# Optimization experiments

Measured on AMD Instinct MI355X. Metric: run time of the kernel, lower is better.

## Reference

```python
import jax, jax.numpy as jnp
import numpy as np
from jax import lax

FILTERS = 8      # Conv1D filters per column
K = 5            # kernel_size
ACTION_DIM = 2
COLS = [16, 128, 1024]  # columns entering each of the 3 blocks (grow x FILTERS)


def setup_inputs() -> dict:
    key = jax.random.key(0)
    ks = jax.random.split(key, 8)
    B, L, C = 64, 128, 16
    state = jax.random.normal(ks[0], (B, L, C), jnp.float32)
    inp = {"state": state}
    # One grouped-conv kernel per block: WIO layout [K, in_per_group=1, cols*FILTERS].
    # Channel c*FILTERS+f of the output is column c's filter f (matches Keras concat order).
    for i, c in enumerate(COLS):
        inp[f"k{i+1}"] = jax.random.normal(ks[1 + i], (K, 1, c * FILTERS), jnp.float32) * 0.1
        inp[f"b{i+1}"] = jnp.zeros((c * FILTERS,), jnp.float32)
    L_final = L - len(COLS) * (K - 1)          # 116
    feat = L_final * COLS[-1] * FILTERS        # 950272
    inp["W"] = jax.random.normal(ks[4], (feat, ACTION_DIM), jnp.float32) * 1e-3
    inp["bd"] = jnp.zeros((ACTION_DIM,), jnp.float32)
    return inp


def _block(x, kern, bias):
    # x: [B, cols, L]  ->  [B, cols*FILTERS, L-K+1]
    cols = x.shape[1]
    xin = jnp.transpose(x, (0, 2, 1))  # [B, L, cols] (NWC)
    y = lax.conv_general_dilated(
        xin, kern, window_strides=(1,), padding='VALID',
        dimension_numbers=('NWC', 'WIO', 'NWC'), feature_group_count=cols)
    y = jax.nn.relu(y + bias)          # [B, L', cols*FILTERS]
    return jnp.transpose(y, (0, 2, 1))


def reference(state, k1, b1, k2, b2, k3, b3, W, bd):
    # Actor.call: transpose [B,L,C] -> [B,C,L], run blocks, transpose back, flatten, dense+tanh
    x = jnp.transpose(state, (0, 2, 1))  # [B, cols=16, L=128]
    for kern, bias in ((k1, b1), (k2, b2), (k3, b3)):
        x = _block(x, kern, bias)
    x = jnp.transpose(x, (0, 2, 1)).reshape(state.shape[0], -1)  # [B, L'*channels]
    return jnp.tanh(x @ W + bd)  # [B, ACTION_DIM]
```

## Files before the change

### kernel.cpp

```cpp
#include <hip/hip_runtime.h>
#include <math.h>

#define NB    64
#define L0    128
#define C0    16
#define KW    5
#define NF    8
#define L1    124
#define L2    120
#define L3    116
#define CH1   128
#define CH2   1024
#define CH3   8192
#define NCHUNK 8
#define NS     4
#define SLICE  29
#define TROWS  (SLICE + 4)
#define Y1R    (SLICE + 8)
#define STR    (SLICE + 12)
#define NFH    4
#define NBATCH 4
#define NBG    (NB / NBATCH)

__global__ __launch_bounds__(256, 2) void actor_fused_kernel(
    const float* __restrict__ state,
    const float* __restrict__ k1,
    const float* __restrict__ b1,
    const float* __restrict__ k2,
    const float* __restrict__ b2,
    const float* __restrict__ k3,
    const float* __restrict__ b3,
    const float* __restrict__ W,
    float* __restrict__ partials)
{
    const int chunk = blockIdx.x;
    const int bg    = blockIdx.y;
    const int slice = blockIdx.z;
    const int t0    = slice * SLICE;
    const int tid   = threadIdx.x;
    const int c3loc = tid >> 1;
    const int fh    = tid & 1;
    const int c3    = chunk * 128 + c3loc;

    __shared__ float s_state[NBATCH][STR][2];
    __shared__ float s_y1[NBATCH][Y1R][16];
    __shared__ float tile[NBATCH][TROWS][128];

    {
        int bb = tid >> 6, lt = tid & 63;
        const float* sp = state + (size_t)(bg * NBATCH + bb) * L0 * C0
                        + (size_t)t0 * C0 + chunk * 2;
        for (int i = lt; i < STR * 2; i += 64) {
            int r = i >> 1, c = i & 1;
            s_state[bb][r][c] = sp[r * C0 + c];
        }
    }
    __syncthreads();

    {
        int bb = tid >> 6, lt = tid & 63;
        for (int i = lt; i < Y1R * 16; i += 64) {
            int r = i >> 4, jloc = i & 15;
            int j = chunk * 16 + jloc;
            int cloc = jloc >> 3;
            float acc = b1[j];
#pragma unroll
            for (int k = 0; k < KW; ++k)
                acc = fmaf(s_state[bb][r + k][cloc], k1[k * CH1 + j], acc);
            s_y1[bb][r][jloc] = fmaxf(acc, 0.f);
        }
    }
    __syncthreads();

    {
        int c = tid & 127, h = tid >> 7;
        int m = chunk * 128 + c;
        int jloc = c >> 3;
        float kk[KW], b2v = b2[m];
#pragma unroll
        for (int k = 0; k < KW; ++k) kk[k] = k2[k * CH2 + m];
        int r0 = h ? 17 : 0, r1 = h ? TROWS : 17;
#pragma unroll
        for (int bb = 0; bb < NBATCH; ++bb)
            for (int r = r0; r < r1; ++r) {
                float acc = b2v;
#pragma unroll
                for (int k = 0; k < KW; ++k)
                    acc = fmaf(s_y1[bb][r + k][jloc], kk[k], acc);
                tile[bb][r][c] = fmaxf(acc, 0.f);
            }
    }

    float kw[KW][NFH], bv[NFH];
#pragma unroll
    for (int k = 0; k < KW; ++k)
#pragma unroll
        for (int f = 0; f < NFH; ++f)
            kw[k][f] = k3[k * CH3 + c3 * NF + fh * NFH + f];
#pragma unroll
    for (int f = 0; f < NFH; ++f)
        bv[f] = b3[c3 * NF + fh * NFH + f];

    __syncthreads();

    float ax[NBATCH], ay[NBATCH];
#pragma unroll
    for (int bb = 0; bb < NBATCH; ++bb) { ax[bb] = 0.f; ay[bb] = 0.f; }

    float w[NBATCH][4];
#pragma unroll
    for (int bb = 0; bb < NBATCH; ++bb)
#pragma unroll
        for (int r = 0; r < 4; ++r)
            w[bb][r] = tile[bb][r][c3loc];

    const float4* __restrict__ wp =
        (const float4*)W + (size_t)t0 * 4096 + (size_t)c3 * 4 + fh * 2;

    for (int t = 0; t < SLICE; ++t) {
        float4 q0 = wp[0];
        float4 q1 = wp[1];
        wp += 4096;

        float v[NBATCH][NFH];
#pragma unroll
        for (int bb = 0; bb < NBATCH; ++bb) {
            float w4 = tile[bb][t + 4][c3loc];
#pragma unroll
            for (int f = 0; f < NFH; ++f) {
                float a = bv[f];
                a = fmaf(w[bb][0], kw[0][f], a);
                a = fmaf(w[bb][1], kw[1][f], a);
                a = fmaf(w[bb][2], kw[2][f], a);
                a = fmaf(w[bb][3], kw[3][f], a);
                a = fmaf(w4,       kw[4][f], a);
                v[bb][f] = fmaxf(a, 0.f);
            }
            w[bb][0] = w[bb][1]; w[bb][1] = w[bb][2];
            w[bb][2] = w[bb][3]; w[bb][3] = w4;
        }

#pragma unroll
        for (int bb = 0; bb < NBATCH; ++bb) {
            ax[bb] = fmaf(v[bb][0], q0.x, ax[bb]); ay[bb] = fmaf(v[bb][0], q0.y, ay[bb]);
            ax[bb] = fmaf(v[bb][1], q0.z, ax[bb]); ay[bb] = fmaf(v[bb][1], q0.w, ay[bb]);
            ax[bb] = fmaf(v[bb][2], q1.x, ax[bb]); ay[bb] = fmaf(v[bb][2], q1.y, ay[bb]);
            ax[bb] = fmaf(v[bb][3], q1.z, ax[bb]); ay[bb] = fmaf(v[bb][3], q1.w, ay[bb]);
        }
    }

#pragma unroll
    for (int bb = 0; bb < NBATCH; ++bb) {
#pragma unroll
        for (int d = 32; d >= 1; d >>= 1) {
            ax[bb] += __shfl_down(ax[bb], d, 64);
            ay[bb] += __shfl_down(ay[bb], d, 64);
        }
    }
    __shared__ float red[4][NBATCH][2];
    int wave = tid >> 6, lane = tid & 63;
    if (lane == 0) {
#pragma unroll
        for (int bb = 0; bb < NBATCH; ++bb) {
            red[wave][bb][0] = ax[bb];
            red[wave][bb][1] = ay[bb];
        }
    }
    __syncthreads();
    if (tid < NBATCH * 2) {
        int bb = tid >> 1, a = tid & 1;
        float s = (red[0][bb][a] + red[1][bb][a]) + (red[2][bb][a] + red[3][bb][a]);
        int b = bg * NBATCH + bb;
        partials[(((size_t)b * NCHUNK + chunk) * NS + slice) * 2 + a] = s;
    }
}

__global__ __launch_bounds__(128) void finish_kernel(
    const float* __restrict__ partials,
    const float* __restrict__ bd,
    float* __restrict__ out)
{
    int i = threadIdx.x;
    int b = i >> 1, a = i & 1;
    float s = bd[a];
#pragma unroll
    for (int p = 0; p < NCHUNK * NS; ++p)
        s += partials[((size_t)b * NCHUNK * NS + p) * 2 + a];
    out[b * 2 + a] = tanhf(s);
}

extern "C" void kernel_launch(void* const* d_in, const int* in_sizes, int n_in,
                              void* d_out, int out_size, void* d_ws, size_t ws_size,
                              hipStream_t stream) {
    const float* state = (const float*)d_in[0];
    const float* k1    = (const float*)d_in[1];
    const float* b1    = (const float*)d_in[2];
    const float* k2    = (const float*)d_in[3];
    const float* b2    = (const float*)d_in[4];
    const float* k3    = (const float*)d_in[5];
    const float* b3    = (const float*)d_in[6];
    const float* W     = (const float*)d_in[7];
    const float* bd    = (const float*)d_in[8];
    float* out = (float*)d_out;

    float* partials = (float*)d_ws;

    dim3 grid(NCHUNK, NBG, NS);
    actor_fused_kernel<<<grid, 256, 0, stream>>>(
        state, k1, b1, k2, b2, k3, b3, W, partials);

    finish_kernel<<<1, 128, 0, stream>>>(partials, bd, out);
}
```

Baseline: 93.06 us.

## Interleave batch dimension into float4 shared-memory tiles and prefetch W one step ahead

Shared-memory tiles now store the four batches of each position as one float4, so layer-2 and layer-3 loops do one 128-bit LDS per row instead of four scalar loads. The batch loop becomes float4 arithmetic, and sliding-window registers are kept across rows in layer 2. The W loads for the next time step are issued one iteration early to hide global-memory latency. The cost is higher per-thread register use, which may pressure the 2-blocks-per-CU occupancy target, and possible bank conflicts on the wider shared-memory accesses.

Result: no change. 92.71 us (-0.4%).

```diff
diff --git a/kernel.cpp b/kernel.cpp
--- a/kernel.cpp
+++ b/kernel.cpp
@@ -6,9 +6,6 @@
 #define C0    16
 #define KW    5
 #define NF    8
-#define L1    124
-#define L2    120
-#define L3    116
 #define CH1   128
 #define CH2   1024
 #define CH3   8192
@@ -21,6 +18,16 @@
 #define NFH    4
 #define NBATCH 4
 #define NBG    (NB / NBATCH)
+
+__device__ __forceinline__ float4 fma4(float4 a, float s, float4 c) {
+    return make_float4(fmaf(a.x, s, c.x), fmaf(a.y, s, c.y),
+                       fmaf(a.z, s, c.z), fmaf(a.w, s, c.w));
+}
+__device__ __forceinline__ float4 relu4(float4 a) {
+    return make_float4(fmaxf(a.x, 0.f), fmaxf(a.y, 0.f),
+                       fmaxf(a.z, 0.f), fmaxf(a.w, 0.f));
+}
+__device__ __forceinline__ float4 splat4(float s) { return make_float4(s, s, s, s); }
 
 __global__ __launch_bounds__(256, 2) void actor_fused_kernel(
     const float* __restrict__ state,
@@ -42,9 +49,9 @@
     const int fh    = tid & 1;
     const int c3    = chunk * 128 + c3loc;
 
-    __shared__ float s_state[NBATCH][STR][2];
-    __shared__ float s_y1[NBATCH][Y1R][16];
-    __shared__ float tile[NBATCH][TROWS][128];
+    __shared__ float  s_state[NBATCH][STR][2];
+    __shared__ float4 s_y1[Y1R][16];
+    __shared__ float4 tile[TROWS][128];
 
     {
         int bb = tid >> 6, lt = tid & 63;
@@ -67,7 +74,7 @@
 #pragma unroll
             for (int k = 0; k < KW; ++k)
                 acc = fmaf(s_state[bb][r + k][cloc], k1[k * CH1 + j], acc);
-            s_y1[bb][r][jloc] = fmaxf(acc, 0.f);
+            ((float*)&s_y1[r][jloc])[bb] = fmaxf(acc, 0.f);
         }
     }
     __syncthreads();
@@ -80,15 +87,21 @@
 #pragma unroll
         for (int k = 0; k < KW; ++k) kk[k] = k2[k * CH2 + m];
         int r0 = h ? 17 : 0, r1 = h ? TROWS : 17;
-#pragma unroll
-        for (int bb = 0; bb < NBATCH; ++bb)
-            for (int r = r0; r < r1; ++r) {
-                float acc = b2v;
-#pragma unroll
-                for (int k = 0; k < KW; ++k)
-                    acc = fmaf(s_y1[bb][r + k][jloc], kk[k], acc);
-                tile[bb][r][c] = fmaxf(acc, 0.f);
-            }
+        float4 u0 = s_y1[r0 + 0][jloc];
+        float4 u1 = s_y1[r0 + 1][jloc];
+        float4 u2 = s_y1[r0 + 2][jloc];
+        float4 u3 = s_y1[r0 + 3][jloc];
+        for (int r = r0; r < r1; ++r) {
+            float4 u4 = s_y1[r + 4][jloc];
+            float4 acc = splat4(b2v);
+            acc = fma4(u0, kk[0], acc);
+            acc = fma4(u1, kk[1], acc);
+            acc = fma4(u2, kk[2], acc);
+            acc = fma4(u3, kk[3], acc);
+            acc = fma4(u4, kk[4], acc);
+            tile[r][c] = relu4(acc);
+            u0 = u1; u1 = u2; u2 = u3; u3 = u4;
+        }
     }
 
     float kw[KW][NFH], bv[NFH];
@@ -103,68 +116,59 @@
 
     __syncthreads();
 
-    float ax[NBATCH], ay[NBATCH];
-#pragma unroll
-    for (int bb = 0; bb < NBATCH; ++bb) { ax[bb] = 0.f; ay[bb] = 0.f; }
-
-    float w[NBATCH][4];
-#pragma unroll
-    for (int bb = 0; bb < NBATCH; ++bb)
-#pragma unroll
-        for (int r = 0; r < 4; ++r)
-            w[bb][r] = tile[bb][r][c3loc];
-
-    const float4* __restrict__ wp =
+    float4 axv = splat4(0.f), ayv = splat4(0.f);
+
+    const float4* __restrict__ wq =
         (const float4*)W + (size_t)t0 * 4096 + (size_t)c3 * 4 + fh * 2;
+    float4 cq0 = wq[0];
+    float4 cq1 = wq[1];
+
+    float4 tw0 = tile[0][c3loc];
+    float4 tw1 = tile[1][c3loc];
+    float4 tw2 = tile[2][c3loc];
+    float4 tw3 = tile[3][c3loc];
 
     for (int t = 0; t < SLICE; ++t) {
-        float4 q0 = wp[0];
-        float4 q1 = wp[1];
-        wp += 4096;
-
-        float v[NBATCH][NFH];
-#pragma unroll
-        for (int bb = 0; bb < NBATCH; ++bb) {
-            float w4 = tile[bb][t + 4][c3loc];
-#pragma unroll
-            for (int f = 0; f < NFH; ++f) {
-                float a = bv[f];
-                a = fmaf(w[bb][0], kw[0][f], a);
-                a = fmaf(w[bb][1], kw[1][f], a);
-                a = fmaf(w[bb][2], kw[2][f], a);
-                a = fmaf(w[bb][3], kw[3][f], a);
-                a = fmaf(w4,       kw[4][f], a);
-                v[bb][f] = fmaxf(a, 0.f);
-            }
-            w[bb][0] = w[bb][1]; w[bb][1] = w[bb][2];
-            w[bb][2] = w[bb][3]; w[bb][3] = w4;
-        }
-
-#pragma unroll
-        for (int bb = 0; bb < NBATCH; ++bb) {
-            ax[bb] = fmaf(v[bb][0], q0.x, ax[bb]); ay[bb] = fmaf(v[bb][0], q0.y, ay[bb]);
-            ax[bb] = fmaf(v[bb][1], q0.z, ax[bb]); ay[bb] = fmaf(v[bb][1], q0.w, ay[bb]);
-            ax[bb] = fmaf(v[bb][2], q1.x, ax[bb]); ay[bb] = fmaf(v[bb][2], q1.y, ay[bb]);
-            ax[bb] = fmaf(v[bb][3], q1.z, ax[bb]); ay[bb] = fmaf(v[bb][3], q1.w, ay[bb]);
-        }
-    }
-
-#pragma unroll
-    for (int bb = 0; bb < NBATCH; ++bb) {
-#pragma unroll
-        for (int d = 32; d >= 1; d >>= 1) {
-            ax[bb] += __shfl_down(ax[bb], d, 64);
-            ay[bb] += __shfl_down(ay[bb], d, 64);
-        }
+        float4 tw4 = tile[t + 4][c3loc];
+        int tp = (t < SLICE - 1) ? (t + 1) : (SLICE - 1);
+        float4 nq0 = wq[(size_t)tp * 4096];
+        float4 nq1 = wq[(size_t)tp * 4096 + 1];
+
+        float4 v[NFH];
+#pragma unroll
+        for (int f = 0; f < NFH; ++f) {
+            float4 a = splat4(bv[f]);
+            a = fma4(tw0, kw[0][f], a);
+            a = fma4(tw1, kw[1][f], a);
+            a = fma4(tw2, kw[2][f], a);
+            a = fma4(tw3, kw[3][f], a);
+            a = fma4(tw4, kw[4][f], a);
+            v[f] = relu4(a);
+        }
+
+        axv = fma4(v[0], cq0.x, axv); ayv = fma4(v[0], cq0.y, ayv);
+        axv = fma4(v[1], cq0.z, axv); ayv = fma4(v[1], cq0.w, ayv);
+        axv = fma4(v[2], cq1.x, axv); ayv = fma4(v[2], cq1.y, ayv);
+        axv = fma4(v[3], cq1.z, axv); ayv = fma4(v[3], cq1.w, ayv);
+
+        cq0 = nq0; cq1 = nq1;
+        tw0 = tw1; tw1 = tw2; tw2 = tw3; tw3 = tw4;
+    }
+
+#pragma unroll
+    for (int d = 32; d >= 1; d >>= 1) {
+        axv.x += __shfl_down(axv.x, d, 64); ayv.x += __shfl_down(ayv.x, d, 64);
+        axv.y += __shfl_down(axv.y, d, 64); ayv.y += __shfl_down(ayv.y, d, 64);
+        axv.z += __shfl_down(axv.z, d, 64); ayv.z += __shfl_down(ayv.z, d, 64);
+        axv.w += __shfl_down(axv.w, d, 64); ayv.w += __shfl_down(ayv.w, d, 64);
     }
     __shared__ float red[4][NBATCH][2];
     int wave = tid >> 6, lane = tid & 63;
     if (lane == 0) {
-#pragma unroll
-        for (int bb = 0; bb < NBATCH; ++bb) {
-            red[wave][bb][0] = ax[bb];
-            red[wave][bb][1] = ay[bb];
-        }
+        red[wave][0][0] = axv.x; red[wave][0][1] = ayv.x;
+        red[wave][1][0] = axv.y; red[wave][1][1] = ayv.y;
+        red[wave][2][0] = axv.z; red[wave][2][1] = ayv.z;
+        red[wave][3][0] = axv.w; red[wave][3][1] = ayv.w;
     }
     __syncthreads();
     if (tid < NBATCH * 2) {
```

## Interleave batch in shared memory as float4 and software-pipeline W loads

Applied to the files above, without the earlier changes.

Shared-memory buffers are re-laid out so the four batch rows of each position sit together as one 4-wide vector. Each conv step then does a single vector LDS read and packed vector FMAs, which could map to the MI355X packed-FP32 instructions. The main loop is unrolled by two, with register rotation, and W loads are prefetched one iteration ahead to hide global latency. The costs are higher register pressure under launch_bounds(256,2) and more complex clamped index logic at the tail.

Result: faster. 90.03 us (median of 2 runs) (-3.3%).

```diff
diff --git a/kernel.cpp b/kernel.cpp
--- a/kernel.cpp
+++ b/kernel.cpp
@@ -6,9 +6,6 @@
 #define C0    16
 #define KW    5
 #define NF    8
-#define L1    124
-#define L2    120
-#define L3    116
 #define CH1   128
 #define CH2   1024
 #define CH3   8192
@@ -21,6 +18,16 @@
 #define NFH    4
 #define NBATCH 4
 #define NBG    (NB / NBATCH)
+
+typedef float v4f __attribute__((ext_vector_type(4)));
+
+__device__ __forceinline__ v4f splat(float s) { return (v4f){s, s, s, s}; }
+__device__ __forceinline__ v4f vfma(v4f a, float s, v4f c) {
+    return __builtin_elementwise_fma(a, splat(s), c);
+}
+__device__ __forceinline__ v4f vrelu(v4f a) {
+    return __builtin_elementwise_max(a, splat(0.f));
+}
 
 __global__ __launch_bounds__(256, 2) void actor_fused_kernel(
     const float* __restrict__ state,
@@ -43,8 +50,8 @@
     const int c3    = chunk * 128 + c3loc;
 
     __shared__ float s_state[NBATCH][STR][2];
-    __shared__ float s_y1[NBATCH][Y1R][16];
-    __shared__ float tile[NBATCH][TROWS][128];
+    __shared__ v4f   s_y1[Y1R][16];
+    __shared__ v4f   tile[TROWS][128];
 
     {
         int bb = tid >> 6, lt = tid & 63;
@@ -67,7 +74,7 @@
 #pragma unroll
             for (int k = 0; k < KW; ++k)
                 acc = fmaf(s_state[bb][r + k][cloc], k1[k * CH1 + j], acc);
-            s_y1[bb][r][jloc] = fmaxf(acc, 0.f);
+            ((float*)&s_y1[r][jloc])[bb] = fmaxf(acc, 0.f);
         }
     }
     __syncthreads();
@@ -79,16 +86,22 @@
         float kk[KW], b2v = b2[m];
 #pragma unroll
         for (int k = 0; k < KW; ++k) kk[k] = k2[k * CH2 + m];
-        int r0 = h ? 17 : 0, r1 = h ? TROWS : 17;
-#pragma unroll
-        for (int bb = 0; bb < NBATCH; ++bb)
-            for (int r = r0; r < r1; ++r) {
-                float acc = b2v;
-#pragma unroll
-                for (int k = 0; k < KW; ++k)
-                    acc = fmaf(s_y1[bb][r + k][jloc], kk[k], acc);
-                tile[bb][r][c] = fmaxf(acc, 0.f);
-            }
+        int r0i = h ? 17 : 0, r1i = h ? TROWS : 17;
+        v4f u0 = s_y1[r0i + 0][jloc];
+        v4f u1 = s_y1[r0i + 1][jloc];
+        v4f u2 = s_y1[r0i + 2][jloc];
+        v4f u3 = s_y1[r0i + 3][jloc];
+        for (int r = r0i; r < r1i; ++r) {
+            v4f u4 = s_y1[r + 4][jloc];
+            v4f acc = splat(b2v);
+            acc = vfma(u0, kk[0], acc);
+            acc = vfma(u1, kk[1], acc);
+            acc = vfma(u2, kk[2], acc);
+            acc = vfma(u3, kk[3], acc);
+            acc = vfma(u4, kk[4], acc);
+            tile[r][c] = vrelu(acc);
+            u0 = u1; u1 = u2; u2 = u3; u3 = u4;
+        }
     }
 
     float kw[KW][NFH], bv[NFH];
@@ -103,60 +116,65 @@
 
     __syncthreads();
 
-    float ax[NBATCH], ay[NBATCH];
-#pragma unroll
-    for (int bb = 0; bb < NBATCH; ++bb) { ax[bb] = 0.f; ay[bb] = 0.f; }
-
-    float w[NBATCH][4];
+    v4f accx = splat(0.f), accy = splat(0.f);
+
+    const v4f* __restrict__ wb =
+        (const v4f*)W + (size_t)t0 * 4096 + (size_t)c3 * 4 + fh * 2;
+    v4f qa0 = wb[0],    qa1 = wb[1];
+    v4f qb0 = wb[4096], qb1 = wb[4097];
+
+    v4f r0 = tile[0][c3loc], r1 = tile[1][c3loc], r2 = tile[2][c3loc],
+        r3 = tile[3][c3loc], r4 = tile[4][c3loc], rn = tile[5][c3loc];
+
+#define SUBITER(A0, A1, A2, A3, A4, Q0, Q1)                                   \
+    {                                                                          \
+        v4f v0 = splat(bv[0]), v1 = splat(bv[1]);                              \
+        v4f v2 = splat(bv[2]), v3 = splat(bv[3]);                              \
+        v0 = vfma(A0, kw[0][0], v0); v1 = vfma(A0, kw[0][1], v1);              \
+        v2 = vfma(A0, kw[0][2], v2); v3 = vfma(A0, kw[0][3], v3);              \
+        v0 = vfma(A1, kw[1][0], v0); v1 = vfma(A1, kw[1][1], v1);              \
+        v2 = vfma(A1, kw[1][2], v2); v3 = vfma(A1, kw[1][3], v3);              \
+        v0 = vfma(A2, kw[2][0], v0); v1 = vfma(A2, kw[2][1], v1);              \
+        v2 = vfma(A2, kw[2][2], v2); v3 = vfma(A2, kw[2][3], v3);              \
+        v0 = vfma(A3, kw[3][0], v0); v1 = vfma(A3, kw[3][1], v1);              \
+        v2 = vfma(A3, kw[3][2], v2); v3 = vfma(A3, kw[3][3], v3);              \
+        v0 = vfma(A4, kw[4][0], v0); v1 = vfma(A4, kw[4][1], v1);              \
+        v2 = vfma(A4, kw[4][2], v2); v3 = vfma(A4, kw[4][3], v3);              \
+        v0 = vrelu(v0); v1 = vrelu(v1); v2 = vrelu(v2); v3 = vrelu(v3);        \
+        accx = vfma(v0, Q0.x, accx); accy = vfma(v0, Q0.y, accy);              \
+        accx = vfma(v1, Q0.z, accx); accy = vfma(v1, Q0.w, accy);              \
+        accx = vfma(v2, Q1.x, accx); accy = vfma(v2, Q1.y, accy);              \
+        accx = vfma(v3, Q1.z, accx); accy = vfma(v3, Q1.w, accy);              \
+    }
+
+    for (int t = 0; t < SLICE - 1; t += 2) {
+        v4f na = tile[t + 6][c3loc];
+        int tb = (t + 7 < TROWS) ? (t + 7) : (TROWS - 1);
+        v4f nb = tile[tb][c3loc];
+
+        SUBITER(r0, r1, r2, r3, r4, qa0, qa1);
+        qa0 = wb[(size_t)(t + 2) * 4096];
+        qa1 = wb[(size_t)(t + 2) * 4096 + 1];
+
+        SUBITER(r1, r2, r3, r4, rn, qb0, qb1);
+        int tp = (t + 3 < SLICE) ? (t + 3) : (SLICE - 1);
+        qb0 = wb[(size_t)tp * 4096];
+        qb1 = wb[(size_t)tp * 4096 + 1];
+
+        r0 = r2; r1 = r3; r2 = r4; r3 = rn; r4 = na; rn = nb;
+    }
+    SUBITER(r0, r1, r2, r3, r4, qa0, qa1);
+#undef SUBITER
+
+    float ax[NBATCH] = {accx.x, accx.y, accx.z, accx.w};
+    float ay[NBATCH] = {accy.x, accy.y, accy.z, accy.w};
 #pragma unroll
     for (int bb = 0; bb < NBATCH; ++bb)
-#pragma unroll
-        for (int r = 0; r < 4; ++r)
-            w[bb][r] = tile[bb][r][c3loc];
-
-    const float4* __restrict__ wp =
-        (const float4*)W + (size_t)t0 * 4096 + (size_t)c3 * 4 + fh * 2;
-
-    for (int t = 0; t < SLICE; ++t) {
-        float4 q0 = wp[0];
-        float4 q1 = wp[1];
-        wp += 4096;
-
-        float v[NBATCH][NFH];
-#pragma unroll
-        for (int bb = 0; bb < NBATCH; ++bb) {
-            float w4 = tile[bb][t + 4][c3loc];
-#pragma unroll
-            for (int f = 0; f < NFH; ++f) {
-                float a = bv[f];
-                a = fmaf(w[bb][0], kw[0][f], a);
-                a = fmaf(w[bb][1], kw[1][f], a);
-                a = fmaf(w[bb][2], kw[2][f], a);
-                a = fmaf(w[bb][3], kw[3][f], a);
-                a = fmaf(w4,       kw[4][f], a);
-                v[bb][f] = fmaxf(a, 0.f);
-            }
-            w[bb][0] = w[bb][1]; w[bb][1] = w[bb][2];
-            w[bb][2] = w[bb][3]; w[bb][3] = w4;
-        }
-
-#pragma unroll
-        for (int bb = 0; bb < NBATCH; ++bb) {
-            ax[bb] = fmaf(v[bb][0], q0.x, ax[bb]); ay[bb] = fmaf(v[bb][0], q0.y, ay[bb]);
-            ax[bb] = fmaf(v[bb][1], q0.z, ax[bb]); ay[bb] = fmaf(v[bb][1], q0.w, ay[bb]);
-            ax[bb] = fmaf(v[bb][2], q1.x, ax[bb]); ay[bb] = fmaf(v[bb][2], q1.y, ay[bb]);
-            ax[bb] = fmaf(v[bb][3], q1.z, ax[bb]); ay[bb] = fmaf(v[bb][3], q1.w, ay[bb]);
-        }
-    }
-
-#pragma unroll
-    for (int bb = 0; bb < NBATCH; ++bb) {
 #pragma unroll
         for (int d = 32; d >= 1; d >>= 1) {
             ax[bb] += __shfl_down(ax[bb], d, 64);
             ay[bb] += __shfl_down(ay[bb], d, 64);
         }
-    }
     __shared__ float red[4][NBATCH][2];
     int wave = tid >> 6, lane = tid & 63;
     if (lane == 0) {
```
